# Optimization experiments

Hardware: AMD Instinct MI355X
Metric: run time of the kernel (lower is better)

## Reference

```python
import jax, jax.numpy as jnp
import numpy as np

MAX_ITER = 3  # matches init max_iter
# structures exercised: sib_be, sib_bb, cop, grd, split (all distinct branches)


def _mfvi(s_const, s_arg_begin, s_arg_end,
          s_sib_be, s_sib_eb, s_sib_bb, s_sib_ee,
          s_cop_b, s_cop_e, s_grd_b, s_grd_e, s_split,
          edge_mask, chart_mask):
    B, S, _ = edge_mask.shape
    idx = jnp.arange(S)
    hs = jnp.broadcast_to(idx[:, None], (S, S))   # hs[i,j] = i (head index)
    ms = jnp.broadcast_to(idx[None, :], (S, S))   # ms[i,j] = j (modifier index)
    ls, rs = jnp.minimum(hs, ms), jnp.maximum(hs, ms)

    c0 = chart_mask[:, 0]
    pad_mask = c0[:, :, None] & c0[:, None, :]           # [B,j,k]
    chart = jnp.roll(chart_mask, 1, axis=1)              # cat((chart[:,-1:], chart[:,:-1]), 1)

    # [B,i,j,k] = edge[b,i,j] & edge[b,i,k]
    mask2o_base = edge_mask[:, :, :, None] & edge_mask[:, :, None, :]
    ne_hk = (hs[:, :, None] != idx)                      # i != k
    mask2o_wm = mask2o_base & ne_hk[None]
    mask2o = mask2o_wm & (ms[:, :, None] != idx)[None]   # additionally j != k

    lhs = ls[None, :, :] >= hs[:, :, None]               # min(j,k) >= i
    rhs = rs[None, :, :] <= hs[:, :, None]               # max(j,k) <= i
    triu_jk = idx[:, None] <= idx[None, :]               # keep k >= j (torch .triu())
    noncross = mask2o_wm & (triu_jk[None, None] & (lhs | rhs)[None])

    span_m2o = (chart[:, :, :, None]
                & (rs[:, :, None] != idx)[None]          # max(i,j) != k
                & pad_mask[:, None, :, :])
    inside = (hs[:, :, None] <= idx) & (ms[:, :, None] >= idx)  # i<=k<=... & j>=k
    outside = (~inside)[None] & span_m2o

    mzero = lambda s, m: jnp.where(m, s, 0.0)
    s_sib_be_m = mzero(s_sib_be, mask2o_wm)
    s_sib_eb_m = mzero(s_sib_eb, jnp.swapaxes(mask2o_wm, -2, -1))
    s_sib_bb_m = mzero(s_sib_bb, mask2o)
    s_sib_ee_m = mzero(s_sib_ee, mask2o)
    s_cop_b_m = mzero(s_cop_b, mask2o)
    s_cop_e_m = mzero(s_cop_e, mask2o)
    s_edge_grd_b = mzero(s_grd_b, noncross)
    s_edge_grd_e = mzero(s_grd_e, jnp.swapaxes(noncross, -2, -1))
    s_span_grd_b = mzero(jnp.transpose(s_grd_b, (0, 2, 3, 1)), outside)
    s_span_grd_e = mzero(jnp.transpose(s_grd_e, (0, 3, 2, 1)), outside)
    s_split_m = mzero(s_split, span_m2o)

    # NOTE: the torch code does `tmp_q_b = s_arg_begin; tmp_q_b += ...`, which
    # mutates the base score tensors in place, so messages ACCUMULATE into the
    # bases across iterations. We reproduce that semantics here.
    base_b, base_e, base_s = s_arg_begin, s_arg_end, s_const
    q_b, q_e, q_s = base_b, base_e, base_s
    for _ in range(MAX_ITER):
        qb = jax.nn.sigmoid(q_b)
        qe = jax.nn.sigmoid(q_e)
        qs = jax.nn.sigmoid(q_s)
        base_b = (base_b
                  + jnp.einsum('bik,bijk->bij', qe, s_sib_be_m)
                  + jnp.einsum('bik,bijk->bij', qb, s_sib_bb_m)
                  + jnp.einsum('bkj,bijk->bij', qb, s_cop_b_m)
                  + jnp.einsum('bjk,bijk->bij', qs, s_edge_grd_b))
        base_e = (base_e
                  + jnp.einsum('bik,bijk->bij', qb, s_sib_eb_m)
                  + jnp.einsum('bik,bijk->bij', qe, s_sib_ee_m)
                  + jnp.einsum('bkj,bijk->bij', qe, s_cop_e_m)
                  + jnp.einsum('bkj,bijk->bij', qs, s_edge_grd_e))
        base_s = (base_s
                  + jnp.einsum('bki,bijk->bij', qb, s_span_grd_b)
                  + jnp.einsum('bkj,bijk->bij', qe, s_span_grd_e)
                  + jnp.einsum('bik,bijk->bij', qs, s_split_m))
        q_b, q_e, q_s = base_b, base_e, base_s
    return q_b, q_e, q_s


def setup_inputs() -> dict:
    key = jax.random.key(0)
    B, S = 4, 128
    ks = jax.random.split(key, 16)
    f3 = lambda k: jax.random.normal(k, (B, S, S), jnp.float32)
    # scale 4D scores down so sums over S stay in a sane sigmoid range
    f4 = lambda k: jax.random.normal(k, (B, S, S, S), jnp.float32) * 0.05
    return {
        's_const': f3(ks[0]),
        's_arg_begin': f3(ks[1]),
        's_arg_end': f3(ks[2]),
        's_sib_be': f4(ks[3]),
        's_sib_eb': f4(ks[4]),
        's_sib_bb': f4(ks[5]),
        's_sib_ee': f4(ks[6]),
        's_cop_b': f4(ks[7]),
        's_cop_e': f4(ks[8]),
        's_grd_b': f4(ks[9]),
        's_grd_e': f4(ks[10]),
        's_split': f4(ks[11]),
        'arg_begin_mask': jax.random.bernoulli(ks[12], 0.5, (B, S, S)),
        'chart_mask': jax.random.bernoulli(ks[13], 0.5, (B, S, S)),
    }


def reference(s_const, s_arg_begin, s_arg_end,
              s_sib_be, s_sib_eb, s_sib_bb, s_sib_ee,
              s_cop_b, s_cop_e, s_grd_b, s_grd_e, s_split,
              arg_begin_mask, chart_mask):
    return _mfvi(s_const, s_arg_begin, s_arg_end,
                 s_sib_be, s_sib_eb, s_sib_bb, s_sib_ee,
                 s_cop_b, s_cop_e, s_grd_b, s_grd_e, s_split,
                 arg_begin_mask, chart_mask)
```

## Files before the change

kernel.cpp:

```cpp
#include <hip/hip_runtime.h>

#define BB 4
#define S 128
#define SS (S*S)
#define BSS (BB*SS)

__device__ __forceinline__ int off3(int b, int i, int j) { return (b * S + i) * S + j; }
__device__ __forceinline__ int off4(int b, int i, int j, int k) { return ((b * S + i) * S + j) * S + k; }

__global__ __launch_bounds__(256) void k_sigmoid(const float* __restrict__ sb,
                                                 const float* __restrict__ se,
                                                 const float* __restrict__ ss,
                                                 float* base,
                                                 float* __restrict__ ws, int init) {
    const int b = blockIdx.z, p = blockIdx.y;
    const int ti = blockIdx.x >> 2, tj = blockIdx.x & 3;
    const int col = threadIdx.x & 31, r0 = threadIdx.x >> 5;
    const float* src = (p == 0) ? sb : (p == 1) ? se : ss;

    __shared__ float tile[32][33];
#pragma unroll
    for (int rr = 0; rr < 4; ++rr) {
        const int row = r0 + 8 * rr;
        const int gi = 32 * ti + row, gj = 32 * tj + col;
        const float x = src[off3(b, gi, gj)];
        const float q = 1.0f / (1.0f + __expf(-x));
        ws[p * BSS + off3(b, gi, gj)] = q;
        if (init) base[p * BSS + off3(b, gi, gj)] = x;
        tile[row][col] = q;
    }
    __syncthreads();
#pragma unroll
    for (int rr = 0; rr < 4; ++rr) {
        const int rowo = r0 + 8 * rr;
        ws[(3 + p) * BSS + off3(b, 32 * tj + rowo, 32 * ti + col)] = tile[col][rowo];
    }
}

__global__ __launch_bounds__(256, 3) void k_terms(
    const float* __restrict__ be, const float* __restrict__ bb,
    const float* __restrict__ cb, const float* __restrict__ eb,
    const float* __restrict__ ee, const float* __restrict__ ce,
    const float* __restrict__ sp, const float* __restrict__ gb,
    const float* __restrict__ ge, const int* __restrict__ edge,
    const int* __restrict__ chart, const float* __restrict__ ws,
    float* __restrict__ base) {
    const int b = blockIdx.z, y = blockIdx.y, x = blockIdx.x;
    const int t = threadIdx.x, hw = t >> 5, lh = t & 31, l = t & 63;
    const int K = 4 * lh;

    const float* qb = ws;
    const float* qe = ws + BSS;
    const float* qs = ws + 2 * BSS;
    const float* qbT = ws + 3 * BSS;
    const float* qeT = ws + 4 * BSS;
    const float* qsT = ws + 5 * BSS;

    if (y < 7) {
        const int I = x;
        const float* A;
        int plane;
        switch (y) {
            case 0: A = be; plane = 0; break;
            case 1: A = bb; plane = 0; break;
            case 2: A = cb; plane = 0; break;
            case 3: A = eb; plane = 1; break;
            case 4: A = ee; plane = 1; break;
            case 5: A = ce; plane = 1; break;
            default: A = sp; plane = 2; break;
        }
        const int Iprev = (I + S - 1) & (S - 1);

        const bool pe0 = edge[off3(b, I, l)] != 0;
        const bool pe1 = edge[off3(b, I, 64 + l)] != 0;
        unsigned long long Mlo = __ballot(pe0), Mhi = __ballot(pe1);
        if (y == 6) {
            const bool pc0 = chart[off3(b, 0, l)] != 0;
            const bool pc1 = chart[off3(b, 0, 64 + l)] != 0;
            const bool ph0 = chart[off3(b, Iprev, l)] != 0;
            const bool ph1 = chart[off3(b, Iprev, 64 + l)] != 0;
            Mlo = __ballot(pc0) & __ballot(ph0);
            Mhi = __ballot(pc1) & __ballot(ph1);
        } else if (y == 3) {
            if (I < 64) Mlo &= ~(1ull << I);
            else Mhi &= ~(1ull << (I - 64));
        }

        const float* qrow = (y == 0 || y == 4) ? qe : (y == 1 || y == 3) ? qb : qs;
        const float4 qv = *(const float4*)&qrow[off3(b, I, K)];
        const int4 ekv = *(const int4*)&edge[off3(b, I, K)];
        const int4 c0kv = *(const int4*)&chart[off3(b, 0, K)];
        float pm[4];
        bool pmask[4];
#pragma unroll
        for (int c = 0; c < 4; ++c) {
            const bool ek = (&ekv.x)[c] != 0;
            const bool c0k = (&c0kv.x)[c] != 0;
            const bool nI = (I != K + c);
            if (y == 0 || y == 1 || y == 4) pm[c] = (ek && nI) ? (&qv.x)[c] : 0.f;
            else if (y == 3) pm[c] = ek ? (&qv.x)[c] : 0.f;
            else if (y == 6) pm[c] = c0k ? (&qv.x)[c] : 0.f;
            pmask[c] = ek && nI;
        }
        const int corrSel = (y == 1 || y == 4) ? 1 : (y == 6) ? 2 : 0;
        const float* qT3 = (y == 2) ? qbT : qeT;

        float acc[16];
        if (y == 2 || y == 5) {
#pragma unroll
            for (int h = 0; h < 2; ++h) {
                float4 va[8], cf[8];
#pragma unroll
                for (int u = 0; u < 8; ++u) {
                    const int j = 8 * (8 * h + u) + hw;
                    va[u] = *(const float4*)&A[off4(b, I, j, K)];
                    cf[u] = *(const float4*)&qT3[off3(b, j, K)];
                }
#pragma unroll
                for (int u = 0; u < 8; ++u) {
                    const int jj = 8 * h + u;
                    const int j = 8 * jj + hw;
                    float dot = 0.f;
                    float s_[4];
#pragma unroll
                    for (int c = 0; c < 4; ++c) {
                        s_[c] = pmask[c] ? (&cf[u].x)[c] : 0.f;
                        dot += s_[c] * (&va[u].x)[c];
                    }
#pragma unroll
                    for (int c = 0; c < 4; ++c)
                        dot -= (K + c == j) ? s_[c] * (&va[u].x)[c] : 0.f;
                    const unsigned long long M = (jj < 8) ? Mlo : Mhi;
                    const bool bit = (M >> (((jj & 7) << 3) + hw)) & 1;
                    acc[jj] = bit ? dot : 0.f;
                }
            }
        } else {
            float4 v[16];
#pragma unroll
            for (int jj = 0; jj < 16; ++jj)
                v[jj] = *(const float4*)&A[off4(b, I, 8 * jj + hw, K)];
#pragma unroll
            for (int jj = 0; jj < 16; ++jj) {
                const int j = 8 * jj + hw;
                float dot = pm[0] * v[jj].x + pm[1] * v[jj].y + pm[2] * v[jj].z + pm[3] * v[jj].w;
                const int ci = (corrSel == 0) ? 256 : (corrSel == 1) ? j : (I > j ? I : j);
#pragma unroll
                for (int c = 0; c < 4; ++c)
                    dot -= (K + c == ci) ? pm[c] * (&v[jj].x)[c] : 0.f;
                const unsigned long long M = (jj < 8) ? Mlo : Mhi;
                const bool bit = (M >> (((jj & 7) << 3) + hw)) & 1;
                acc[jj] = bit ? dot : 0.f;
            }
        }

#pragma unroll
        for (int o = 16; o > 0; o >>= 1) {
#pragma unroll
            for (int jj = 0; jj < 16; ++jj) acc[jj] += __shfl_xor(acc[jj], o);
        }
        if (lh == 0) {
#pragma unroll
            for (int jj = 0; jj < 16; ++jj)
                atomicAdd(&base[plane * BSS + off3(b, I, 8 * jj + hw)], acc[jj]);
        }
    } else {
        const float* A = (y == 7) ? gb : ge;
        const float* qT = (y == 7) ? qbT : qeT;
        const int Jt = x & 15, Is = x >> 4;
        const int J = 8 * Jt + hw, I0 = 16 * Is;

        const float4 q_J = (y == 7) ? *(const float4*)&qs[off3(b, J, K)]
                                    : *(const float4*)&qsT[off3(b, J, K)];
        const int4 c0Kv = *(const int4*)&chart[off3(b, 0, K)];
        const bool c0J = chart[off3(b, 0, J)] != 0;
        const int Jprev = (J + S - 1) & (S - 1);
        const int4 chJKv = *(const int4*)&chart[off3(b, Jprev, K)];
        bool c0K[4], chJK[4], chKJ[4];
        int mxJ[4];
#pragma unroll
        for (int c = 0; c < 4; ++c) {
            c0K[c] = (&c0Kv.x)[c] != 0;
            chJK[c] = (&chJKv.x)[c] != 0;
            chKJ[c] = (y == 8) ? (chart[off3(b, (K + c + S - 1) & (S - 1), J)] != 0) : false;
            mxJ[c] = J > (K + c) ? J : (K + c);
        }

        const unsigned long long MeIJ = __ballot(edge[off3(b, I0 + (l & 15), J)] != 0);
        const unsigned long long Mc0I = __ballot(chart[off3(b, 0, I0 + (l & 15))] != 0);
        const int hsh = l & 32;

        float4 qtv[4];
#pragma unroll
        for (int q4 = 0; q4 < 4; ++q4)
            qtv[q4] = *(const float4*)&qT[off3(b, J, I0 + 4 * q4)];

        float accE[16];
        float rs[4] = {0.f, 0.f, 0.f, 0.f};

#pragma unroll
        for (int hf = 0; hf < 2; ++hf) {
            float4 v[8];
            int4 ev[8];
#pragma unroll
            for (int u = 0; u < 8; ++u) {
                const int I = I0 + 8 * hf + u;
                v[u] = *(const float4*)&A[off4(b, I, J, K)];
                ev[u] = *(const int4*)&edge[off3(b, I, K)];
            }
#pragma unroll
            for (int u = 0; u < 8; ++u) {
                const int s = 8 * hf + u;
                const int I = I0 + s;
                const bool eIJ = (MeIJ >> (hsh + s)) & 1;
                const bool c0I = (Mc0I >> (hsh + s)) & 1;
                const float qT_JI = (&qtv[s >> 2].x)[s & 3];

                float p_ = 0.f;
#pragma unroll
                for (int c = 0; c < 4; ++c) {
                    const int Kc = K + c;
                    const bool eIK = (&ev[u].x)[c] != 0;
                    const float vv = (&v[u].x)[c];
                    bool nc, o;
                    if (y == 7) {
                        nc = eIJ && eIK && (I != Kc) && (J <= Kc) && (J >= I || Kc <= I);
                        o = !((J <= I) && (Kc >= I)) && chJK[c] && (mxJ[c] != I) && c0K[c] && c0I;
                    } else {
                        nc = eIK && eIJ && (I != J) && (Kc <= J) && (Kc >= I || J <= I);
                        o = !((Kc <= I) && (J >= I)) && chKJ[c] && (mxJ[c] != I) && c0J && c0I;
                    }
                    p_ += (nc ? (&q_J.x)[c] : 0.f) * vv;
                    rs[c] += (o ? qT_JI : 0.f) * vv;
                }
                accE[s] = p_;
            }
        }

#pragma unroll
        for (int o = 16; o > 0; o >>= 1) {
#pragma unroll
            for (int s = 0; s < 16; ++s) accE[s] += __shfl_xor(accE[s], o);
        }
        if (lh == 0) {
#pragma unroll
            for (int s = 0; s < 16; ++s)
                atomicAdd(&base[(y == 7 ? 0 : 1) * BSS + off3(b, I0 + s, J)], accE[s]);
        }

#pragma unroll
        for (int c = 0; c < 4; ++c) {
            if (y == 7)
                atomicAdd(&base[2 * BSS + off3(b, J, K + c)], rs[c]);
            else
                atomicAdd(&base[2 * BSS + off3(b, K + c, J)], rs[c]);
        }
    }
}

extern "C" void kernel_launch(void* const* d_in, const int* in_sizes, int n_in,
                              void* d_out, int out_size, void* d_ws, size_t ws_size,
                              hipStream_t stream) {
    (void)in_sizes; (void)n_in; (void)out_size; (void)ws_size;
    const float* s_const = (const float*)d_in[0];
    const float* s_arg_begin = (const float*)d_in[1];
    const float* s_arg_end = (const float*)d_in[2];
    const float* be = (const float*)d_in[3];
    const float* eb = (const float*)d_in[4];
    const float* bb = (const float*)d_in[5];
    const float* ee = (const float*)d_in[6];
    const float* cb = (const float*)d_in[7];
    const float* ce = (const float*)d_in[8];
    const float* gb = (const float*)d_in[9];
    const float* ge = (const float*)d_in[10];
    const float* sp = (const float*)d_in[11];
    const int* edge = (const int*)d_in[12];
    const int* chart = (const int*)d_in[13];
    float* base = (float*)d_out;
    float* ws = (float*)d_ws;

    for (int it = 0; it < 3; ++it) {
        if (it == 0)
            k_sigmoid<<<dim3(16, 3, BB), dim3(256), 0, stream>>>(s_arg_begin, s_arg_end,
                                                                 s_const, base, ws, 1);
        else
            k_sigmoid<<<dim3(16, 3, BB), dim3(256), 0, stream>>>(base, base + BSS,
                                                                 base + 2 * BSS, base, ws, 0);
        k_terms<<<dim3(S, 9, BB), dim3(256), 0, stream>>>(be, bb, cb, eb, ee, ce, sp, gb, ge,
                                                          edge, chart, ws, base);
    }
}
```

Measured before the change: 465.0 us.

## Process two units per block with software-prefetched loads of next unit

The grid collapses to a 1D launch where each block handles two consecutive rows (or two J tiles for the guard terms). Loads for the second unit are issued before the first unit's reduction and atomics, so memory latency overlaps with shuffle and atomic work. The guard branch also packs the edge mask into a 64-bit bitmask loaded once and reused across both units. The cost is more live registers and half as many blocks, which may lower occupancy.

After: 961.0 us. 107% more time.

```diff
diff --git a/kernel.cpp b/kernel.cpp
--- a/kernel.cpp
+++ b/kernel.cpp
@@ -45,7 +45,6 @@
     const float* __restrict__ ge, const int* __restrict__ edge,
     const int* __restrict__ chart, const float* __restrict__ ws,
     float* __restrict__ base) {
-    const int b = blockIdx.z, y = blockIdx.y, x = blockIdx.x;
     const int t = threadIdx.x, hw = t >> 5, lh = t & 31, l = t & 63;
     const int K = 4 * lh;
 
@@ -56,8 +55,11 @@
     const float* qeT = ws + 4 * BSS;
     const float* qsT = ws + 5 * BSS;
 
-    if (y < 7) {
-        const int I = x;
+    if (blockIdx.x < 1792) {
+        const int u0 = 2 * blockIdx.x;
+        const int y = u0 >> 9;
+        const int b = (u0 >> 7) & 3;
+        const int I0 = u0 & 127;
         const float* A;
         int plane;
         switch (y) {
@@ -69,191 +71,237 @@
             case 5: A = ce; plane = 1; break;
             default: A = sp; plane = 2; break;
         }
-        const int Iprev = (I + S - 1) & (S - 1);
-
-        const bool pe0 = edge[off3(b, I, l)] != 0;
-        const bool pe1 = edge[off3(b, I, 64 + l)] != 0;
-        unsigned long long Mlo = __ballot(pe0), Mhi = __ballot(pe1);
+        const bool is25 = (y == 2 || y == 5);
+        const float* qrow = (y == 0 || y == 4) ? qe : (y == 1 || y == 3) ? qb : qs;
+        const float* qT3 = (y == 2) ? qbT : qeT;
+        const int corrSel = (y == 1 || y == 4) ? 1 : (y == 6) ? 2 : 0;
+
+        unsigned long long C0lo = 0, C0hi = 0;
+        int4 c0kv = make_int4(0, 0, 0, 0);
         if (y == 6) {
-            const bool pc0 = chart[off3(b, 0, l)] != 0;
-            const bool pc1 = chart[off3(b, 0, 64 + l)] != 0;
-            const bool ph0 = chart[off3(b, Iprev, l)] != 0;
-            const bool ph1 = chart[off3(b, Iprev, 64 + l)] != 0;
-            Mlo = __ballot(pc0) & __ballot(ph0);
-            Mhi = __ballot(pc1) & __ballot(ph1);
-        } else if (y == 3) {
-            if (I < 64) Mlo &= ~(1ull << I);
-            else Mhi &= ~(1ull << (I - 64));
-        }
-
-        const float* qrow = (y == 0 || y == 4) ? qe : (y == 1 || y == 3) ? qb : qs;
-        const float4 qv = *(const float4*)&qrow[off3(b, I, K)];
-        const int4 ekv = *(const int4*)&edge[off3(b, I, K)];
-        const int4 c0kv = *(const int4*)&chart[off3(b, 0, K)];
-        float pm[4];
-        bool pmask[4];
-#pragma unroll
-        for (int c = 0; c < 4; ++c) {
-            const bool ek = (&ekv.x)[c] != 0;
-            const bool c0k = (&c0kv.x)[c] != 0;
-            const bool nI = (I != K + c);
-            if (y == 0 || y == 1 || y == 4) pm[c] = (ek && nI) ? (&qv.x)[c] : 0.f;
-            else if (y == 3) pm[c] = ek ? (&qv.x)[c] : 0.f;
-            else if (y == 6) pm[c] = c0k ? (&qv.x)[c] : 0.f;
-            pmask[c] = ek && nI;
-        }
-        const int corrSel = (y == 1 || y == 4) ? 1 : (y == 6) ? 2 : 0;
-        const float* qT3 = (y == 2) ? qbT : qeT;
-
-        float acc[16];
-        if (y == 2 || y == 5) {
-#pragma unroll
-            for (int h = 0; h < 2; ++h) {
-                float4 va[8], cf[8];
-#pragma unroll
-                for (int u = 0; u < 8; ++u) {
-                    const int j = 8 * (8 * h + u) + hw;
-                    va[u] = *(const float4*)&A[off4(b, I, j, K)];
-                    cf[u] = *(const float4*)&qT3[off3(b, j, K)];
+            C0lo = __ballot(chart[off3(b, 0, l)] != 0);
+            C0hi = __ballot(chart[off3(b, 0, 64 + l)] != 0);
+            c0kv = *(const int4*)&chart[off3(b, 0, K)];
+        }
+        float4 cf[16];
+        if (is25) {
+#pragma unroll
+            for (int jj = 0; jj < 16; ++jj)
+                cf[jj] = *(const float4*)&qT3[off3(b, 8 * jj + hw, K)];
+        }
+
+        float4 v[16];
+        int eLoN = 0, eHiN = 0, phLoN = 0, phHiN = 0;
+        float4 qvN = make_float4(0.f, 0.f, 0.f, 0.f);
+        int4 ekvN = make_int4(0, 0, 0, 0);
+
+        auto issue_unit = [&](int I) {
+#pragma unroll
+            for (int jj = 0; jj < 16; ++jj)
+                v[jj] = *(const float4*)&A[off4(b, I, 8 * jj + hw, K)];
+            ekvN = *(const int4*)&edge[off3(b, I, K)];
+            if (y == 6) {
+                const int Ip = (I + S - 1) & (S - 1);
+                phLoN = chart[off3(b, Ip, l)];
+                phHiN = chart[off3(b, Ip, 64 + l)];
+            } else {
+                eLoN = edge[off3(b, I, l)];
+                eHiN = edge[off3(b, I, 64 + l)];
+            }
+            if (!is25) qvN = *(const float4*)&qrow[off3(b, I, K)];
+        };
+
+        issue_unit(I0);
+#pragma unroll 1
+        for (int k = 0; k < 2; ++k) {
+            const int I = I0 + k;
+            unsigned long long Mlo, Mhi;
+            if (y == 6) {
+                Mlo = C0lo & __ballot(phLoN != 0);
+                Mhi = C0hi & __ballot(phHiN != 0);
+            } else {
+                Mlo = __ballot(eLoN != 0);
+                Mhi = __ballot(eHiN != 0);
+                if (y == 3) {
+                    if (I < 64) Mlo &= ~(1ull << I);
+                    else Mhi &= ~(1ull << (I - 64));
                 }
-#pragma unroll
-                for (int u = 0; u < 8; ++u) {
-                    const int jj = 8 * h + u;
+            }
+            float pm[4];
+            bool em[4];
+#pragma unroll
+            for (int c = 0; c < 4; ++c) {
+                const bool ek = (&ekvN.x)[c] != 0;
+                const bool c0k = (&c0kv.x)[c] != 0;
+                const bool nI = (I != K + c);
+                em[c] = ek && nI;
+                if (y == 0 || y == 1 || y == 4) pm[c] = em[c] ? (&qvN.x)[c] : 0.f;
+                else if (y == 3) pm[c] = ek ? (&qvN.x)[c] : 0.f;
+                else if (y == 6) pm[c] = c0k ? (&qvN.x)[c] : 0.f;
+                else pm[c] = 0.f;
+            }
+
+            float acc[16];
+            if (is25) {
+#pragma unroll
+                for (int jj = 0; jj < 16; ++jj) {
                     const int j = 8 * jj + hw;
                     float dot = 0.f;
-                    float s_[4];
 #pragma unroll
                     for (int c = 0; c < 4; ++c) {
-                        s_[c] = pmask[c] ? (&cf[u].x)[c] : 0.f;
-                        dot += s_[c] * (&va[u].x)[c];
+                        const float term = (&cf[jj].x)[c] * (&v[jj].x)[c];
+                        dot += (em[c] && (K + c != j)) ? term : 0.f;
                     }
+                    acc[jj] = dot;
+                }
+            } else {
+#pragma unroll
+                for (int jj = 0; jj < 16; ++jj) {
+                    const int j = 8 * jj + hw;
+                    float dot = pm[0] * v[jj].x + pm[1] * v[jj].y + pm[2] * v[jj].z +
+                                pm[3] * v[jj].w;
+                    const int ci = (corrSel == 0) ? 256 : (corrSel == 1) ? j : (I > j ? I : j);
 #pragma unroll
                     for (int c = 0; c < 4; ++c)
-                        dot -= (K + c == j) ? s_[c] * (&va[u].x)[c] : 0.f;
-                    const unsigned long long M = (jj < 8) ? Mlo : Mhi;
-                    const bool bit = (M >> (((jj & 7) << 3) + hw)) & 1;
-                    acc[jj] = bit ? dot : 0.f;
+                        dot -= (K + c == ci) ? pm[c] * (&v[jj].x)[c] : 0.f;
+                    acc[jj] = dot;
                 }
             }
-        } else {
-            float4 v[16];
-#pragma unroll
-            for (int jj = 0; jj < 16; ++jj)
-                v[jj] = *(const float4*)&A[off4(b, I, 8 * jj + hw, K)];
+
+            if (k < 1) issue_unit(I0 + 1);
+
 #pragma unroll
             for (int jj = 0; jj < 16; ++jj) {
-                const int j = 8 * jj + hw;
-                float dot = pm[0] * v[jj].x + pm[1] * v[jj].y + pm[2] * v[jj].z + pm[3] * v[jj].w;
-                const int ci = (corrSel == 0) ? 256 : (corrSel == 1) ? j : (I > j ? I : j);
+                const bool bit = (((jj < 8) ? Mlo : Mhi) >> (((jj & 7) << 3) + hw)) & 1;
+                acc[jj] = bit ? acc[jj] : 0.f;
+            }
+#pragma unroll
+            for (int o = 16; o > 0; o >>= 1) {
+#pragma unroll
+                for (int jj = 0; jj < 16; ++jj) acc[jj] += __shfl_xor(acc[jj], o);
+            }
+            if (lh == 0) {
+#pragma unroll
+                for (int jj = 0; jj < 16; ++jj)
+                    atomicAdd(&base[plane * BSS + off3(b, I, 8 * jj + hw)], acc[jj]);
+            }
+        }
+    } else {
+        const int bx7 = blockIdx.x - 1792;
+        const int u0 = 2 * bx7;
+        const int y8 = u0 >> 9;
+        const int b = (u0 >> 7) & 3;
+        const int x7 = u0 & 127;
+        const int Jt0 = x7 & 15;
+        const int Is = x7 >> 4;
+        const int I0 = 16 * Is;
+        const float* A = (y8 == 0) ? gb : ge;
+        const float* qT = (y8 == 0) ? qbT : qeT;
+        const float* qJsrc = (y8 == 0) ? qs : qsT;
+        const int hsh = l & 32;
+
+        const unsigned long long Mc0I = __ballot(chart[off3(b, 0, I0 + (l & 15))] != 0);
+        const int4 c0Kv = *(const int4*)&chart[off3(b, 0, K)];
+        bool c0K[4];
+#pragma unroll
+        for (int c = 0; c < 4; ++c) c0K[c] = (&c0Kv.x)[c] != 0;
+        unsigned long long ebits = 0ull;
+#pragma unroll
+        for (int s = 0; s < 16; ++s) {
+            const int4 e4 = *(const int4*)&edge[off3(b, I0 + s, K)];
+#pragma unroll
+            for (int c = 0; c < 4; ++c)
+                if ((&e4.x)[c] != 0) ebits |= (1ull << (4 * s + c));
+        }
+
+        float4 v[16];
+        float4 q_JN = make_float4(0.f, 0.f, 0.f, 0.f);
+        float4 qtvN[4];
+        int eColJN = 0;
+        int4 chJKvN = make_int4(0, 0, 0, 0);
+        int c0JN = 0;
+        int chKJN[4] = {0, 0, 0, 0};
+
+        auto issue_unit7 = [&](int J) {
+#pragma unroll
+            for (int s = 0; s < 16; ++s)
+                v[s] = *(const float4*)&A[off4(b, I0 + s, J, K)];
+            q_JN = *(const float4*)&qJsrc[off3(b, J, K)];
+#pragma unroll
+            for (int q4 = 0; q4 < 4; ++q4)
+                qtvN[q4] = *(const float4*)&qT[off3(b, J, I0 + 4 * q4)];
+            eColJN = edge[off3(b, I0 + (l & 15), J)];
+            const int Jprev = (J + S - 1) & (S - 1);
+            chJKvN = *(const int4*)&chart[off3(b, Jprev, K)];
+            c0JN = chart[off3(b, 0, J)];
+            if (y8 == 1) {
 #pragma unroll
                 for (int c = 0; c < 4; ++c)
-                    dot -= (K + c == ci) ? pm[c] * (&v[jj].x)[c] : 0.f;
-                const unsigned long long M = (jj < 8) ? Mlo : Mhi;
-                const bool bit = (M >> (((jj & 7) << 3) + hw)) & 1;
-                acc[jj] = bit ? dot : 0.f;
-            }
-        }
-
-#pragma unroll
-        for (int o = 16; o > 0; o >>= 1) {
-#pragma unroll
-            for (int jj = 0; jj < 16; ++jj) acc[jj] += __shfl_xor(acc[jj], o);
-        }
-        if (lh == 0) {
-#pragma unroll
-            for (int jj = 0; jj < 16; ++jj)
-                atomicAdd(&base[plane * BSS + off3(b, I, 8 * jj + hw)], acc[jj]);
-        }
-    } else {
-        const float* A = (y == 7) ? gb : ge;
-        const float* qT = (y == 7) ? qbT : qeT;
-        const int Jt = x & 15, Is = x >> 4;
-        const int J = 8 * Jt + hw, I0 = 16 * Is;
-
-        const float4 q_J = (y == 7) ? *(const float4*)&qs[off3(b, J, K)]
-                                    : *(const float4*)&qsT[off3(b, J, K)];
-        const int4 c0Kv = *(const int4*)&chart[off3(b, 0, K)];
-        const bool c0J = chart[off3(b, 0, J)] != 0;
-        const int Jprev = (J + S - 1) & (S - 1);
-        const int4 chJKv = *(const int4*)&chart[off3(b, Jprev, K)];
-        bool c0K[4], chJK[4], chKJ[4];
-        int mxJ[4];
-#pragma unroll
-        for (int c = 0; c < 4; ++c) {
-            c0K[c] = (&c0Kv.x)[c] != 0;
-            chJK[c] = (&chJKv.x)[c] != 0;
-            chKJ[c] = (y == 8) ? (chart[off3(b, (K + c + S - 1) & (S - 1), J)] != 0) : false;
-            mxJ[c] = J > (K + c) ? J : (K + c);
-        }
-
-        const unsigned long long MeIJ = __ballot(edge[off3(b, I0 + (l & 15), J)] != 0);
-        const unsigned long long Mc0I = __ballot(chart[off3(b, 0, I0 + (l & 15))] != 0);
-        const int hsh = l & 32;
-
-        float4 qtv[4];
-#pragma unroll
-        for (int q4 = 0; q4 < 4; ++q4)
-            qtv[q4] = *(const float4*)&qT[off3(b, J, I0 + 4 * q4)];
-
-        float accE[16];
-        float rs[4] = {0.f, 0.f, 0.f, 0.f};
-
-#pragma unroll
-        for (int hf = 0; hf < 2; ++hf) {
-            float4 v[8];
-            int4 ev[8];
-#pragma unroll
-            for (int u = 0; u < 8; ++u) {
-                const int I = I0 + 8 * hf + u;
-                v[u] = *(const float4*)&A[off4(b, I, J, K)];
-                ev[u] = *(const int4*)&edge[off3(b, I, K)];
-            }
-#pragma unroll
-            for (int u = 0; u < 8; ++u) {
-                const int s = 8 * hf + u;
+                    chKJN[c] = chart[off3(b, (K + c + S - 1) & (S - 1), J)];
+            }
+        };
+
+        issue_unit7(8 * Jt0 + hw);
+#pragma unroll 1
+        for (int k = 0; k < 2; ++k) {
+            const int J = 8 * (Jt0 + k) + hw;
+            const unsigned long long MeIJ = __ballot(eColJN != 0);
+            const bool c0J = c0JN != 0;
+            bool chJK[4], chKJ[4];
+#pragma unroll
+            for (int c = 0; c < 4; ++c) {
+                chJK[c] = (&chJKvN.x)[c] != 0;
+                chKJ[c] = (y8 == 1) ? (chKJN[c] != 0) : false;
+            }
+
+            float accE[16];
+            float rs[4] = {0.f, 0.f, 0.f, 0.f};
+#pragma unroll
+            for (int s = 0; s < 16; ++s) {
                 const int I = I0 + s;
                 const bool eIJ = (MeIJ >> (hsh + s)) & 1;
                 const bool c0I = (Mc0I >> (hsh + s)) & 1;
-                const float qT_JI = (&qtv[s >> 2].x)[s & 3];
-
+                const float qT_JI = (&qtvN[s >> 2].x)[s & 3];
                 float p_ = 0.f;
 #pragma unroll
                 for (int c = 0; c < 4; ++c) {
                     const int Kc = K + c;
-                    const bool eIK = (&ev[u].x)[c] != 0;
-                    const float vv = (&v[u].x)[c];
+                    const bool eIK = (ebits >> (4 * s + c)) & 1;
+                    const float vv = (&v[s].x)[c];
+                    const int mx = J > Kc ? J : Kc;
                     bool nc, o;
-                    if (y == 7) {
+                    if (y8 == 0) {
                         nc = eIJ && eIK && (I != Kc) && (J <= Kc) && (J >= I || Kc <= I);
-                        o = !((J <= I) && (Kc >= I)) && chJK[c] && (mxJ[c] != I) && c0K[c] && c0I;
+                        o = !((J <= I) && (Kc >= I)) && chJK[c] && (mx != I) && c0K[c] && c0I;
                     } else {
                         nc = eIK && eIJ && (I != J) && (Kc <= J) && (Kc >= I || J <= I);
-                        o = !((Kc <= I) && (J >= I)) && chKJ[c] && (mxJ[c] != I) && c0J && c0I;
+                        o = !((Kc <= I) && (J >= I)) && chKJ[c] && (mx != I) && c0J && c0I;
                     }
-                    p_ += (nc ? (&q_J.x)[c] : 0.f) * vv;
+                    p_ += (nc ? (&q_JN.x)[c] : 0.f) * vv;
                     rs[c] += (o ? qT_JI : 0.f) * vv;
                 }
                 accE[s] = p_;
             }
-        }
-
-#pragma unroll
-        for (int o = 16; o > 0; o >>= 1) {
-#pragma unroll
-            for (int s = 0; s < 16; ++s) accE[s] += __shfl_xor(accE[s], o);
-        }
-        if (lh == 0) {
-#pragma unroll
-            for (int s = 0; s < 16; ++s)
-                atomicAdd(&base[(y == 7 ? 0 : 1) * BSS + off3(b, I0 + s, J)], accE[s]);
-        }
-
-#pragma unroll
-        for (int c = 0; c < 4; ++c) {
-            if (y == 7)
-                atomicAdd(&base[2 * BSS + off3(b, J, K + c)], rs[c]);
-            else
-                atomicAdd(&base[2 * BSS + off3(b, K + c, J)], rs[c]);
+
+            if (k < 1) issue_unit7(8 * (Jt0 + 1) + hw);
+
+#pragma unroll
+            for (int o = 16; o > 0; o >>= 1) {
+#pragma unroll
+                for (int s = 0; s < 16; ++s) accE[s] += __shfl_xor(accE[s], o);
+            }
+            if (lh == 0) {
+#pragma unroll
+                for (int s = 0; s < 16; ++s)
+                    atomicAdd(&base[(y8 == 0 ? 0 : 1) * BSS + off3(b, I0 + s, J)], accE[s]);
+            }
+#pragma unroll
+            for (int c = 0; c < 4; ++c) {
+                if (y8 == 0)
+                    atomicAdd(&base[2 * BSS + off3(b, J, K + c)], rs[c]);
+                else
+                    atomicAdd(&base[2 * BSS + off3(b, K + c, J)], rs[c]);
+            }
         }
     }
 }
@@ -286,7 +334,7 @@
         else
             k_sigmoid<<<dim3(16, 3, BB), dim3(256), 0, stream>>>(base, base + BSS,
                                                                  base + 2 * BSS, base, ws, 0);
-        k_terms<<<dim3(S, 9, BB), dim3(256), 0, stream>>>(be, bb, cb, eb, ee, ce, sp, gb, ge,
-                                                          edge, chart, ws, base);
+        k_terms<<<dim3(2304), dim3(256), 0, stream>>>(be, bb, cb, eb, ee, ce, sp, gb, ge,
+                                                      edge, chart, ws, base);
     }
 }
```

## Replace atomic accumulation with per-term workspace planes reduced in sigmoid pass

Applied to the files above, without the earlier changes.

Instead of atomically adding each term's contributions into the output, the edge and span kernels now write partial results to separate workspace planes. The following sigmoid pass sums them. The span kernel is split out and each block handles 32 rows instead of 16, which halves its grid and the number of row-sum partials. The aim is to remove atomic contention and make the result deterministic. The cost is extra workspace traffic, one more kernel launch per iteration, and a final reduction pass.

Result: slower. 565.5 us (+21.6%).

```diff
diff --git a/kernel.cpp b/kernel.cpp
--- a/kernel.cpp
+++ b/kernel.cpp
@@ -5,30 +5,56 @@
 #define SS (S*S)
 #define BSS (BB*SS)
 
+#define WPY0 6
+#define WAE0 13
+#define WAE1 14
+#define WRS0 15
+
 __device__ __forceinline__ int off3(int b, int i, int j) { return (b * S + i) * S + j; }
 __device__ __forceinline__ int off4(int b, int i, int j, int k) { return ((b * S + i) * S + j) * S + k; }
 
 __global__ __launch_bounds__(256) void k_sigmoid(const float* __restrict__ sb,
                                                  const float* __restrict__ se,
                                                  const float* __restrict__ ss,
-                                                 float* base,
-                                                 float* __restrict__ ws, int init) {
+                                                 float* __restrict__ base,
+                                                 float* __restrict__ ws, int mode) {
     const int b = blockIdx.z, p = blockIdx.y;
     const int ti = blockIdx.x >> 2, tj = blockIdx.x & 3;
     const int col = threadIdx.x & 31, r0 = threadIdx.x >> 5;
-    const float* src = (p == 0) ? sb : (p == 1) ? se : ss;
-
     __shared__ float tile[32][33];
+    float* bp = base + p * BSS;
+
 #pragma unroll
     for (int rr = 0; rr < 4; ++rr) {
         const int row = r0 + 8 * rr;
         const int gi = 32 * ti + row, gj = 32 * tj + col;
-        const float x = src[off3(b, gi, gj)];
-        const float q = 1.0f / (1.0f + __expf(-x));
-        ws[p * BSS + off3(b, gi, gj)] = q;
-        if (init) base[p * BSS + off3(b, gi, gj)] = x;
-        tile[row][col] = q;
-    }
+        const int idx = off3(b, gi, gj);
+        float v;
+        if (mode == 0) {
+            const float* src = (p == 0) ? sb : (p == 1) ? se : ss;
+            v = src[idx];
+        } else {
+            v = bp[idx];
+            if (p == 0) {
+                v += ws[(WPY0 + 0) * BSS + idx] + ws[(WPY0 + 1) * BSS + idx] +
+                     ws[(WPY0 + 2) * BSS + idx] + ws[WAE0 * BSS + idx];
+            } else if (p == 1) {
+                v += ws[(WPY0 + 3) * BSS + idx] + ws[(WPY0 + 4) * BSS + idx] +
+                     ws[(WPY0 + 5) * BSS + idx] + ws[WAE1 * BSS + idx];
+            } else {
+                v += ws[(WPY0 + 6) * BSS + idx];
+#pragma unroll
+                for (int n = 0; n < 8; ++n) v += ws[(WRS0 + n) * BSS + idx];
+            }
+        }
+        bp[idx] = v;
+        if (mode < 2) {
+            const float q = 1.0f / (1.0f + __expf(-v));
+            ws[p * BSS + idx] = q;
+            tile[row][col] = q;
+        }
+    }
+    if (mode == 2) return;
     __syncthreads();
 #pragma unroll
     for (int rr = 0; rr < 4; ++rr) {
@@ -37,158 +63,176 @@
     }
 }
 
-__global__ __launch_bounds__(256, 3) void k_terms(
+__global__ __launch_bounds__(256, 3) void k_edge(
     const float* __restrict__ be, const float* __restrict__ bb,
     const float* __restrict__ cb, const float* __restrict__ eb,
     const float* __restrict__ ee, const float* __restrict__ ce,
-    const float* __restrict__ sp, const float* __restrict__ gb,
-    const float* __restrict__ ge, const int* __restrict__ edge,
-    const int* __restrict__ chart, const float* __restrict__ ws,
-    float* __restrict__ base) {
+    const float* __restrict__ sp, const int* __restrict__ edge,
+    const int* __restrict__ chart, float* __restrict__ ws) {
     const int b = blockIdx.z, y = blockIdx.y, x = blockIdx.x;
     const int t = threadIdx.x, hw = t >> 5, lh = t & 31, l = t & 63;
     const int K = 4 * lh;
+    __shared__ float rowbuf[128];
 
     const float* qb = ws;
     const float* qe = ws + BSS;
     const float* qs = ws + 2 * BSS;
     const float* qbT = ws + 3 * BSS;
     const float* qeT = ws + 4 * BSS;
-    const float* qsT = ws + 5 * BSS;
-
-    if (y < 7) {
-        const int I = x;
-        const float* A;
-        int plane;
-        switch (y) {
-            case 0: A = be; plane = 0; break;
-            case 1: A = bb; plane = 0; break;
-            case 2: A = cb; plane = 0; break;
-            case 3: A = eb; plane = 1; break;
-            case 4: A = ee; plane = 1; break;
-            case 5: A = ce; plane = 1; break;
-            default: A = sp; plane = 2; break;
-        }
-        const int Iprev = (I + S - 1) & (S - 1);
-
-        const bool pe0 = edge[off3(b, I, l)] != 0;
-        const bool pe1 = edge[off3(b, I, 64 + l)] != 0;
-        unsigned long long Mlo = __ballot(pe0), Mhi = __ballot(pe1);
-        if (y == 6) {
-            const bool pc0 = chart[off3(b, 0, l)] != 0;
-            const bool pc1 = chart[off3(b, 0, 64 + l)] != 0;
-            const bool ph0 = chart[off3(b, Iprev, l)] != 0;
-            const bool ph1 = chart[off3(b, Iprev, 64 + l)] != 0;
-            Mlo = __ballot(pc0) & __ballot(ph0);
-            Mhi = __ballot(pc1) & __ballot(ph1);
-        } else if (y == 3) {
-            if (I < 64) Mlo &= ~(1ull << I);
-            else Mhi &= ~(1ull << (I - 64));
-        }
-
-        const float* qrow = (y == 0 || y == 4) ? qe : (y == 1 || y == 3) ? qb : qs;
-        const float4 qv = *(const float4*)&qrow[off3(b, I, K)];
-        const int4 ekv = *(const int4*)&edge[off3(b, I, K)];
-        const int4 c0kv = *(const int4*)&chart[off3(b, 0, K)];
-        float pm[4];
-        bool pmask[4];
-#pragma unroll
-        for (int c = 0; c < 4; ++c) {
-            const bool ek = (&ekv.x)[c] != 0;
-            const bool c0k = (&c0kv.x)[c] != 0;
-            const bool nI = (I != K + c);
-            if (y == 0 || y == 1 || y == 4) pm[c] = (ek && nI) ? (&qv.x)[c] : 0.f;
-            else if (y == 3) pm[c] = ek ? (&qv.x)[c] : 0.f;
-            else if (y == 6) pm[c] = c0k ? (&qv.x)[c] : 0.f;
-            pmask[c] = ek && nI;
-        }
-        const int corrSel = (y == 1 || y == 4) ? 1 : (y == 6) ? 2 : 0;
-        const float* qT3 = (y == 2) ? qbT : qeT;
-
-        float acc[16];
-        if (y == 2 || y == 5) {
-#pragma unroll
-            for (int h = 0; h < 2; ++h) {
-                float4 va[8], cf[8];
-#pragma unroll
-                for (int u = 0; u < 8; ++u) {
-                    const int j = 8 * (8 * h + u) + hw;
-                    va[u] = *(const float4*)&A[off4(b, I, j, K)];
-                    cf[u] = *(const float4*)&qT3[off3(b, j, K)];
+
+    const int I = x;
+    const float* A;
+    switch (y) {
+        case 0: A = be; break;
+        case 1: A = bb; break;
+        case 2: A = cb; break;
+        case 3: A = eb; break;
+        case 4: A = ee; break;
+        case 5: A = ce; break;
+        default: A = sp; break;
+    }
+    const int Iprev = (I + S - 1) & (S - 1);
+
+    const bool pe0 = edge[off3(b, I, l)] != 0;
+    const bool pe1 = edge[off3(b, I, 64 + l)] != 0;
+    unsigned long long Mlo = __ballot(pe0), Mhi = __ballot(pe1);
+    if (y == 6) {
+        const bool pc0 = chart[off3(b, 0, l)] != 0;
+        const bool pc1 = chart[off3(b, 0, 64 + l)] != 0;
+        const bool ph0 = chart[off3(b, Iprev, l)] != 0;
+        const bool ph1 = chart[off3(b, Iprev, 64 + l)] != 0;
+        Mlo = __ballot(pc0) & __ballot(ph0);
+        Mhi = __ballot(pc1) & __ballot(ph1);
+    } else if (y == 3) {
+        if (I < 64) Mlo &= ~(1ull << I);
+        else Mhi &= ~(1ull << (I - 64));
+    }
+
+    const float* qrow = (y == 0 || y == 4) ? qe : (y == 1 || y == 3) ? qb : qs;
+    const float4 qv = *(const float4*)&qrow[off3(b, I, K)];
+    const int4 ekv = *(const int4*)&edge[off3(b, I, K)];
+    const int4 c0kv = *(const int4*)&chart[off3(b, 0, K)];
+    float pm[4];
+    bool pmask[4];
+#pragma unroll
+    for (int c = 0; c < 4; ++c) {
+        const bool ek = (&ekv.x)[c] != 0;
+        const bool c0k = (&c0kv.x)[c] != 0;
+        const bool nI = (I != K + c);
+        if (y == 0 || y == 1 || y == 4) pm[c] = (ek && nI) ? (&qv.x)[c] : 0.f;
+        else if (y == 3) pm[c] = ek ? (&qv.x)[c] : 0.f;
+        else if (y == 6) pm[c] = c0k ? (&qv.x)[c] : 0.f;
+        pmask[c] = ek && nI;
+    }
+    const int corrSel = (y == 1 || y == 4) ? 1 : (y == 6) ? 2 : 0;
+    const float* qT3 = (y == 2) ? qbT : qeT;
+
+    float acc[16];
+    if (y == 2 || y == 5) {
+#pragma unroll
+        for (int h = 0; h < 2; ++h) {
+            float4 va[8], cf[8];
+#pragma unroll
+            for (int u = 0; u < 8; ++u) {
+                const int j = 8 * (8 * h + u) + hw;
+                va[u] = *(const float4*)&A[off4(b, I, j, K)];
+                cf[u] = *(const float4*)&qT3[off3(b, j, K)];
+            }
+#pragma unroll
+            for (int u = 0; u < 8; ++u) {
+                const int jj = 8 * h + u;
+                const int j = 8 * jj + hw;
+                float dot = 0.f;
+                float s_[4];
+#pragma unroll
+                for (int c = 0; c < 4; ++c) {
+                    s_[c] = pmask[c] ? (&cf[u].x)[c] : 0.f;
+                    dot += s_[c] * (&va[u].x)[c];
                 }
 #pragma unroll
-                for (int u = 0; u < 8; ++u) {
-                    const int jj = 8 * h + u;
-                    const int j = 8 * jj + hw;
-                    float dot = 0.f;
-                    float s_[4];
-#pragma unroll
-                    for (int c = 0; c < 4; ++c) {
-                        s_[c] = pmask[c] ? (&cf[u].x)[c] : 0.f;
-                        dot += s_[c] * (&va[u].x)[c];
-                    }
-#pragma unroll
-                    for (int c = 0; c < 4; ++c)
-                        dot -= (K + c == j) ? s_[c] * (&va[u].x)[c] : 0.f;
-                    const unsigned long long M = (jj < 8) ? Mlo : Mhi;
-                    const bool bit = (M >> (((jj & 7) << 3) + hw)) & 1;
-                    acc[jj] = bit ? dot : 0.f;
-                }
-            }
-        } else {
-            float4 v[16];
-#pragma unroll
-            for (int jj = 0; jj < 16; ++jj)
-                v[jj] = *(const float4*)&A[off4(b, I, 8 * jj + hw, K)];
-#pragma unroll
-            for (int jj = 0; jj < 16; ++jj) {
-                const int j = 8 * jj + hw;
-                float dot = pm[0] * v[jj].x + pm[1] * v[jj].y + pm[2] * v[jj].z + pm[3] * v[jj].w;
-                const int ci = (corrSel == 0) ? 256 : (corrSel == 1) ? j : (I > j ? I : j);
-#pragma unroll
                 for (int c = 0; c < 4; ++c)
-                    dot -= (K + c == ci) ? pm[c] * (&v[jj].x)[c] : 0.f;
+                    dot -= (K + c == j) ? s_[c] * (&va[u].x)[c] : 0.f;
                 const unsigned long long M = (jj < 8) ? Mlo : Mhi;
                 const bool bit = (M >> (((jj & 7) << 3) + hw)) & 1;
                 acc[jj] = bit ? dot : 0.f;
             }
         }
-
-#pragma unroll
-        for (int o = 16; o > 0; o >>= 1) {
-#pragma unroll
-            for (int jj = 0; jj < 16; ++jj) acc[jj] += __shfl_xor(acc[jj], o);
-        }
-        if (lh == 0) {
-#pragma unroll
-            for (int jj = 0; jj < 16; ++jj)
-                atomicAdd(&base[plane * BSS + off3(b, I, 8 * jj + hw)], acc[jj]);
-        }
     } else {
-        const float* A = (y == 7) ? gb : ge;
-        const float* qT = (y == 7) ? qbT : qeT;
-        const int Jt = x & 15, Is = x >> 4;
-        const int J = 8 * Jt + hw, I0 = 16 * Is;
-
-        const float4 q_J = (y == 7) ? *(const float4*)&qs[off3(b, J, K)]
-                                    : *(const float4*)&qsT[off3(b, J, K)];
-        const int4 c0Kv = *(const int4*)&chart[off3(b, 0, K)];
-        const bool c0J = chart[off3(b, 0, J)] != 0;
-        const int Jprev = (J + S - 1) & (S - 1);
-        const int4 chJKv = *(const int4*)&chart[off3(b, Jprev, K)];
-        bool c0K[4], chJK[4], chKJ[4];
-        int mxJ[4];
-#pragma unroll
-        for (int c = 0; c < 4; ++c) {
-            c0K[c] = (&c0Kv.x)[c] != 0;
-            chJK[c] = (&chJKv.x)[c] != 0;
-            chKJ[c] = (y == 8) ? (chart[off3(b, (K + c + S - 1) & (S - 1), J)] != 0) : false;
-            mxJ[c] = J > (K + c) ? J : (K + c);
-        }
+        float4 v[16];
+#pragma unroll
+        for (int jj = 0; jj < 16; ++jj)
+            v[jj] = *(const float4*)&A[off4(b, I, 8 * jj + hw, K)];
+#pragma unroll
+        for (int jj = 0; jj < 16; ++jj) {
+            const int j = 8 * jj + hw;
+            float dot = pm[0] * v[jj].x + pm[1] * v[jj].y + pm[2] * v[jj].z + pm[3] * v[jj].w;
+            const int ci = (corrSel == 0) ? 256 : (corrSel == 1) ? j : (I > j ? I : j);
+#pragma unroll
+            for (int c = 0; c < 4; ++c)
+                dot -= (K + c == ci) ? pm[c] * (&v[jj].x)[c] : 0.f;
+            const unsigned long long M = (jj < 8) ? Mlo : Mhi;
+            const bool bit = (M >> (((jj & 7) << 3) + hw)) & 1;
+            acc[jj] = bit ? dot : 0.f;
+        }
+    }
+
+#pragma unroll
+    for (int o = 16; o > 0; o >>= 1) {
+#pragma unroll
+        for (int jj = 0; jj < 16; ++jj) acc[jj] += __shfl_xor(acc[jj], o);
+    }
+    if (lh == 0) {
+#pragma unroll
+        for (int jj = 0; jj < 16; ++jj) rowbuf[8 * jj + hw] = acc[jj];
+    }
+    __syncthreads();
+    if (t < 32)
+        *(float4*)&ws[(WPY0 + y) * BSS + off3(b, I, 4 * t)] = *(const float4*)&rowbuf[4 * t];
+}
+
+__global__ __launch_bounds__(256, 3) void k_span(
+    const float* __restrict__ gb, const float* __restrict__ ge,
+    const int* __restrict__ edge, const int* __restrict__ chart,
+    float* __restrict__ ws) {
+    const int b = blockIdx.z, y8 = blockIdx.y, x = blockIdx.x;
+    const int t = threadIdx.x, hw = t >> 5, lh = t & 31, l = t & 63;
+    const int K = 4 * lh;
+
+    const float* qs = ws + 2 * BSS;
+    const float* qbT = ws + 3 * BSS;
+    const float* qeT = ws + 4 * BSS;
+    const float* qsT = ws + 5 * BSS;
+
+    const float* A = (y8 == 0) ? gb : ge;
+    const float* qT = (y8 == 0) ? qbT : qeT;
+    const int Jt = x & 15, Is2 = x >> 4;
+    const int J = 8 * Jt + hw;
+    const int hsh = l & 32;
+
+    const float4 q_J = (y8 == 0) ? *(const float4*)&qs[off3(b, J, K)]
+                                 : *(const float4*)&qsT[off3(b, J, K)];
+    const int4 c0Kv = *(const int4*)&chart[off3(b, 0, K)];
+    const bool c0J = chart[off3(b, 0, J)] != 0;
+    const int Jprev = (J + S - 1) & (S - 1);
+    const int4 chJKv = *(const int4*)&chart[off3(b, Jprev, K)];
+    bool c0K[4], chJK[4], chKJ[4];
+    int mxJ[4];
+#pragma unroll
+    for (int c = 0; c < 4; ++c) {
+        c0K[c] = (&c0Kv.x)[c] != 0;
+        chJK[c] = (&chJKv.x)[c] != 0;
+        chKJ[c] = (y8 == 1) ? (chart[off3(b, (K + c + S - 1) & (S - 1), J)] != 0) : false;
+        mxJ[c] = J > (K + c) ? J : (K + c);
+    }
+
+    float rs[4] = {0.f, 0.f, 0.f, 0.f};
+
+#pragma unroll
+    for (int h = 0; h < 2; ++h) {
+        const int I0 = 32 * Is2 + 16 * h;
 
         const unsigned long long MeIJ = __ballot(edge[off3(b, I0 + (l & 15), J)] != 0);
         const unsigned long long Mc0I = __ballot(chart[off3(b, 0, I0 + (l & 15))] != 0);
-        const int hsh = l & 32;
 
         float4 qtv[4];
 #pragma unroll
@@ -196,8 +240,6 @@
             qtv[q4] = *(const float4*)&qT[off3(b, J, I0 + 4 * q4)];
 
         float accE[16];
-        float rs[4] = {0.f, 0.f, 0.f, 0.f};
-
 #pragma unroll
         for (int hf = 0; hf < 2; ++hf) {
             float4 v[8];
@@ -223,7 +265,7 @@
                     const bool eIK = (&ev[u].x)[c] != 0;
                     const float vv = (&v[u].x)[c];
                     bool nc, o;
-                    if (y == 7) {
+                    if (y8 == 0) {
                         nc = eIJ && eIK && (I != Kc) && (J <= Kc) && (J >= I || Kc <= I);
                         o = !((J <= I) && (Kc >= I)) && chJK[c] && (mxJ[c] != I) && c0K[c] && c0I;
                     } else {
@@ -245,16 +287,17 @@
         if (lh == 0) {
 #pragma unroll
             for (int s = 0; s < 16; ++s)
-                atomicAdd(&base[(y == 7 ? 0 : 1) * BSS + off3(b, I0 + s, J)], accE[s]);
-        }
-
-#pragma unroll
-        for (int c = 0; c < 4; ++c) {
-            if (y == 7)
-                atomicAdd(&base[2 * BSS + off3(b, J, K + c)], rs[c]);
-            else
-                atomicAdd(&base[2 * BSS + off3(b, K + c, J)], rs[c]);
-        }
+                ws[((y8 == 0) ? WAE0 : WAE1) * BSS + off3(b, I0 + s, J)] = accE[s];
+        }
+    }
+
+    if (y8 == 0) {
+        *(float4*)&ws[(WRS0 + Is2) * BSS + off3(b, J, K)] =
+            make_float4(rs[0], rs[1], rs[2], rs[3]);
+    } else {
+#pragma unroll
+        for (int c = 0; c < 4; ++c)
+            ws[(WRS0 + 4 + Is2) * BSS + off3(b, K + c, J)] = rs[c];
     }
 }
 
@@ -280,13 +323,12 @@
     float* ws = (float*)d_ws;
 
     for (int it = 0; it < 3; ++it) {
-        if (it == 0)
-            k_sigmoid<<<dim3(16, 3, BB), dim3(256), 0, stream>>>(s_arg_begin, s_arg_end,
-                                                                 s_const, base, ws, 1);
-        else
-            k_sigmoid<<<dim3(16, 3, BB), dim3(256), 0, stream>>>(base, base + BSS,
-                                                                 base + 2 * BSS, base, ws, 0);
-        k_terms<<<dim3(S, 9, BB), dim3(256), 0, stream>>>(be, bb, cb, eb, ee, ce, sp, gb, ge,
-                                                          edge, chart, ws, base);
-    }
+        k_sigmoid<<<dim3(16, 3, BB), dim3(256), 0, stream>>>(s_arg_begin, s_arg_end, s_const,
+                                                             base, ws, it == 0 ? 0 : 1);
+        k_edge<<<dim3(S, 7, BB), dim3(256), 0, stream>>>(be, bb, cb, eb, ee, ce, sp,
+                                                         edge, chart, ws);
+        k_span<<<dim3(64, 2, BB), dim3(256), 0, stream>>>(gb, ge, edge, chart, ws);
+    }
+    k_sigmoid<<<dim3(16, 3, BB), dim3(256), 0, stream>>>(s_arg_begin, s_arg_end, s_const,
+                                                         base, ws, 2);
 }
```
